# Optimization experiments

Measured on AMD Instinct MI355X. Metric: run time of the kernel, lower is better.

## Reference

```python
import jax, jax.numpy as jnp
import numpy as np

N, E, F, H, HEADS, L, G, NC = 50000, 800000, 128, 64, 4, 3, 64, 2
EPS = 1e-5


def _init(key, shape, fan_in):
    return jax.random.normal(key, shape, jnp.float32) / np.sqrt(fan_in)


def setup_inputs() -> dict:
    key = jax.random.key(0)
    ks = jax.random.split(key, 24)
    x = jax.random.normal(ks[0], (N, F), jnp.float32)
    edge_index = jax.random.randint(ks[1], (2, E), 0, N, jnp.int32)
    batch = jnp.sort(jax.random.randint(ks[2], (N,), 0, G, jnp.int32))
    return {
        "x": x, "edge_index": edge_index, "batch": batch,
        "Wi": _init(ks[3], (F, H), F), "bi": jnp.zeros((H,), jnp.float32),
        "gcn_W": _init(ks[4], (L, H, H), H), "gcn_b": jnp.zeros((L, H), jnp.float32),
        "gcn_gamma": jnp.ones((L, H), jnp.float32), "gcn_beta": jnp.zeros((L, H), jnp.float32),
        "Wg": _init(ks[5], (H, HEADS * H), H), "bg": jnp.zeros((H,), jnp.float32),
        "att_src": _init(ks[6], (HEADS, H), H), "att_dst": _init(ks[7], (HEADS, H), H),
        "gat_gamma": jnp.ones((H,), jnp.float32), "gat_beta": jnp.zeros((H,), jnp.float32),
        "c1_W": _init(ks[8], (2 * H, H), 2 * H), "c1_b": jnp.zeros((H,), jnp.float32),
        "c2_W": _init(ks[9], (H, H // 2), H), "c2_b": jnp.zeros((H // 2,), jnp.float32),
        "c3_W": _init(ks[10], (H // 2, NC), H // 2), "c3_b": jnp.zeros((NC,), jnp.float32),
    }


def _batch_norm(x, gamma, beta):
    # training-mode BN over the node dimension
    mu = x.mean(0)
    var = x.var(0)
    return (x - mu) * jax.lax.rsqrt(var + EPS) * gamma + beta


def _gcn_conv(x, W, b, src, dst):
    # PyG GCNConv: add self loops + symmetric normalization D^-1/2 (A+I) D^-1/2
    h = x @ W  # [N, H]
    ones = jnp.ones((src.shape[0],), h.dtype)
    deg = jax.ops.segment_sum(ones, dst, num_segments=N) + 1.0  # +1 for self loop
    dinv = jax.lax.rsqrt(deg)
    norm = dinv[src] * dinv[dst]  # [E]
    out = jax.ops.segment_sum(h[src] * norm[:, None], dst, num_segments=N)
    out = out + h * (dinv * dinv)[:, None]  # self-loop term: deg^-1
    return out + b


def _gat_conv(x, W, att_s, att_d, b, src, dst):
    # PyG GATConv, concat=False (mean over heads), leaky_relu slope 0.2, self loops
    h = (x @ W).reshape(N, HEADS, H)  # [N, Hd, C]
    a_s = (h * att_s).sum(-1)  # [N, Hd]
    a_d = (h * att_d).sum(-1)
    sl = jnp.arange(N, dtype=src.dtype)
    si = jnp.concatenate([src, sl])
    di = jnp.concatenate([dst, sl])
    logits = jax.nn.leaky_relu(a_s[si] + a_d[di], 0.2)  # [E+N, Hd]
    # segment softmax over destination node per head
    m = jax.ops.segment_max(logits, di, num_segments=N)  # every node has a self loop
    e = jnp.exp(logits - m[di])
    s = jax.ops.segment_sum(e, di, num_segments=N)
    alpha = e / (s[di] + 1e-16)  # [E+N, Hd]
    out = jax.ops.segment_sum(h[si] * alpha[:, :, None], di, num_segments=N)  # [N, Hd, C]
    return out.mean(axis=1) + b


def reference(x, edge_index, batch, Wi, bi, gcn_W, gcn_b, gcn_gamma, gcn_beta,
              Wg, bg, att_src, att_dst, gat_gamma, gat_beta,
              c1_W, c1_b, c2_W, c2_b, c3_W, c3_b):
    src, dst = edge_index[0], edge_index[1]
    h = jax.nn.relu(x @ Wi + bi)
    for l in range(L):
        identity = h
        h = _gcn_conv(h, gcn_W[l], gcn_b[l], src, dst)
        h = _batch_norm(h, gcn_gamma[l], gcn_beta[l])
        h = jax.nn.relu(h)  # dropout: eval mode (identity)
        h = h + identity
    identity = h
    h = _gat_conv(h, Wg, att_src, att_dst, bg, src, dst)
    h = _batch_norm(h, gat_gamma, gat_beta)
    h = jax.nn.elu(h)
    h = h + identity
    # dual pooling over graphs
    cnt = jax.ops.segment_sum(jnp.ones((N,), h.dtype), batch, num_segments=G,
                              indices_are_sorted=True)
    x_mean = jax.ops.segment_sum(h, batch, num_segments=G, indices_are_sorted=True)
    x_mean = x_mean / jnp.maximum(cnt, 1.0)[:, None]
    x_max = jax.ops.segment_max(h, batch, num_segments=G, indices_are_sorted=True)
    x_max = jnp.where(jnp.isfinite(x_max), x_max, 0.0)
    z = jnp.concatenate([x_mean, x_max], axis=1)  # [G, 2H]
    z = jax.nn.relu(z @ c1_W + c1_b)
    z = jax.nn.relu(z @ c2_W + c2_b)
    return z @ c3_W + c3_b  # [G, NC]
```

## Files before the change

kernel.cpp:

```cpp
#include <hip/hip_runtime.h>
#include <math.h>

#define N_ 50000
#define E_ 800000
#define F_ 128
#define H_ 64
#define G_ 64
#define NC_ 2
#define CAP_ 96
#define EPS_ 1e-5f
#define GRID_P 1250
#define GRID_G 2048
#define WIS_STRIDE 136
#define W0_STRIDE 72
#define WGS 72

typedef _Float16 f16;
typedef f16 f16x2 __attribute__((ext_vector_type(2)));
typedef f16 f16x4 __attribute__((ext_vector_type(4)));
typedef f16 f16x8 __attribute__((ext_vector_type(8)));

__device__ __forceinline__ unsigned fkey(float f) {
    unsigned u = __float_as_uint(f);
    return (u & 0x80000000u) ? ~u : (u | 0x80000000u);
}
__device__ __forceinline__ float funkey(unsigned k) {
    unsigned u = (k & 0x80000000u) ? (k & 0x7fffffffu) : ~k;
    return __uint_as_float(u);
}
__device__ __forceinline__ float leaky(float x) { return x > 0.f ? x : 0.2f * x; }

__device__ __forceinline__ void dot8(const f16x8 w, const f16x8 v,
                                     float& a0, float& a1, float& a2, float& a3) {
    a0 = __builtin_amdgcn_fdot2(__builtin_shufflevector(w, w, 0, 1),
                                __builtin_shufflevector(v, v, 0, 1), a0, false);
    a1 = __builtin_amdgcn_fdot2(__builtin_shufflevector(w, w, 2, 3),
                                __builtin_shufflevector(v, v, 2, 3), a1, false);
    a2 = __builtin_amdgcn_fdot2(__builtin_shufflevector(w, w, 4, 5),
                                __builtin_shufflevector(v, v, 4, 5), a2, false);
    a3 = __builtin_amdgcn_fdot2(__builtin_shufflevector(w, w, 6, 7),
                                __builtin_shufflevector(v, v, 6, 7), a3, false);
}

__device__ __forceinline__ int sel4(int4 v, int i) {
    return i == 0 ? v.x : i == 1 ? v.y : i == 2 ? v.z : v.w;
}

__global__ void k_fill(const int* __restrict__ ei, int* __restrict__ rowcnt,
                       int* __restrict__ slotS) {
    int e = blockIdx.x * 256 + threadIdx.x;
    if (e >= E_) return;
    int d = ei[E_ + e];
    int pos = atomicAdd(&rowcnt[d], 1);
    if (pos < CAP_) slotS[d * CAP_ + pos] = ei[e];
}

__global__ __launch_bounds__(256) void k_in_mm(const float* __restrict__ x,
                                               const float* __restrict__ Wi,
                                               const float* __restrict__ bi,
                                               const float* __restrict__ W0,
                                               const int* __restrict__ rowcnt,
                                               float* __restrict__ hA,
                                               f16* __restrict__ hWs) {
    __shared__ __attribute__((aligned(16))) f16 Wis[H_ * WIS_STRIDE];
    __shared__ __attribute__((aligned(16))) f16 W0s[H_ * W0_STRIDE];
    __shared__ __attribute__((aligned(16))) f16 xb[4 * F_];
    __shared__ __attribute__((aligned(16))) f16 rb[4 * H_];
    int tid = threadIdx.x;
    for (int i = tid; i < F_ * H_; i += 256) {
        int k = i >> 6, j = i & 63;
        Wis[j * WIS_STRIDE + k] = (f16)Wi[i];
    }
    for (int i = tid; i < H_ * H_; i += 256) {
        int k = i >> 6, j = i & 63;
        W0s[j * W0_STRIDE + k] = (f16)W0[i];
    }
    __syncthreads();
    int r = tid >> 6, j = tid & 63;
    float bj = bi[j];
    const f16* wc1 = Wis + j * WIS_STRIDE;
    const f16* wc2 = W0s + j * W0_STRIDE;
    f16* xr = xb + r * F_;
    f16* rr = rb + r * H_;
    int grp = blockIdx.x;
    float2 xv = *(const float2*)&x[(size_t)(grp * 4 + r) * F_ + 2 * j];
    for (; grp < N_ / 4; grp += GRID_P) {
        f16x2 xs = {(f16)xv.x, (f16)xv.y};
        *(f16x2*)&xr[2 * j] = xs;
        int ng = grp + GRID_P;
        if (ng < N_ / 4)
            xv = *(const float2*)&x[(size_t)(ng * 4 + r) * F_ + 2 * j];
        int n = grp * 4 + r;
        float a0 = 0.f, a1 = 0.f, a2 = 0.f, a3 = 0.f;
#pragma unroll
        for (int k = 0; k < F_; k += 8)
            dot8(*(const f16x8*)&wc1[k], *(const f16x8*)&xr[k], a0, a1, a2, a3);
        float y = fmaxf((a0 + a1) + (a2 + a3) + bj, 0.f);
        hA[(size_t)n * H_ + j] = y;
        rr[j] = (f16)y;
        float b0 = 0.f, b1 = 0.f, b2 = 0.f, b3 = 0.f;
#pragma unroll
        for (int k = 0; k < H_; k += 8)
            dot8(*(const f16x8*)&wc2[k], *(const f16x8*)&rr[k], b0, b1, b2, b3);
        hWs[(size_t)n * H_ + j] =
            (f16)(((b0 + b1) + (b2 + b3)) * rsqrtf((float)rowcnt[n] + 1.f));
    }
}

__global__ __launch_bounds__(256) void k_gcn_gather(const int* __restrict__ rowcnt,
                                                    const int* __restrict__ slotS,
                                                    const f16* __restrict__ hWs,
                                                    float* __restrict__ out,
                                                    float* __restrict__ bnpart) {
    __shared__ float st[128];
    for (int i = threadIdx.x; i < 128; i += 256) st[i] = 0.f;
    __syncthreads();
    int L = threadIdx.x & 63;
    int rg = L >> 4, q = L & 15;
    for (int grp = blockIdx.x; grp < N_ / 4; grp += GRID_G) {
        int d = grp * 4 + (threadIdx.x >> 6);
        int rc = rowcnt[d];
        int cnt = min(rc, CAP_);
        float dd = rsqrtf((float)rc + 1.f);
        size_t base = (size_t)d * CAP_;
        float a0 = 0.f, a1 = 0.f, a2 = 0.f, a3 = 0.f;
        if (rg == 0) {
            f16x4 hv = *(const f16x4*)&hWs[(size_t)d * H_ + q * 4];
            a0 = (float)hv[0]; a1 = (float)hv[1]; a2 = (float)hv[2]; a3 = (float)hv[3];
        }
        for (int k = 0; k < cnt; k += 16) {
            int4 iA = *(const int4*)&slotS[base + k];
            int4 iB = *(const int4*)&slotS[base + k + 4];
            int4 iC = *(const int4*)&slotS[base + k + 8];
            int4 iD = *(const int4*)&slotS[base + k + 12];
            int e = k + rg;
            int s0 = (e < cnt) ? sel4(iA, rg) : d;
            int s1 = (e + 4 < cnt) ? sel4(iB, rg) : d;
            int s2 = (e + 8 < cnt) ? sel4(iC, rg) : d;
            int s3 = (e + 12 < cnt) ? sel4(iD, rg) : d;
            f16x4 v0 = *(const f16x4*)&hWs[(size_t)s0 * H_ + q * 4];
            f16x4 v1 = *(const f16x4*)&hWs[(size_t)s1 * H_ + q * 4];
            f16x4 v2 = *(const f16x4*)&hWs[(size_t)s2 * H_ + q * 4];
            f16x4 v3 = *(const f16x4*)&hWs[(size_t)s3 * H_ + q * 4];
            float m0 = (e < cnt) ? 1.f : 0.f;
            float m1 = (e + 4 < cnt) ? 1.f : 0.f;
            float m2 = (e + 8 < cnt) ? 1.f : 0.f;
            float m3 = (e + 12 < cnt) ? 1.f : 0.f;
            a0 += (m0 * (float)v0[0] + m1 * (float)v1[0]) +
                  (m2 * (float)v2[0] + m3 * (float)v3[0]);
            a1 += (m0 * (float)v0[1] + m1 * (float)v1[1]) +
                  (m2 * (float)v2[1] + m3 * (float)v3[1]);
            a2 += (m0 * (float)v0[2] + m1 * (float)v1[2]) +
                  (m2 * (float)v2[2] + m3 * (float)v3[2]);
            a3 += (m0 * (float)v0[3] + m1 * (float)v1[3]) +
                  (m2 * (float)v2[3] + m3 * (float)v3[3]);
        }
        a0 += __shfl_xor(a0, 16); a0 += __shfl_xor(a0, 32);
        a1 += __shfl_xor(a1, 16); a1 += __shfl_xor(a1, 32);
        a2 += __shfl_xor(a2, 16); a2 += __shfl_xor(a2, 32);
        a3 += __shfl_xor(a3, 16); a3 += __shfl_xor(a3, 32);
        if (rg == 0) {
            float y0 = a0 * dd, y1 = a1 * dd, y2 = a2 * dd, y3 = a3 * dd;
            *(float4*)&out[(size_t)d * H_ + q * 4] = make_float4(y0, y1, y2, y3);
            atomicAdd(&st[q * 4 + 0], y0);        atomicAdd(&st[64 + q * 4 + 0], y0 * y0);
            atomicAdd(&st[q * 4 + 1], y1);        atomicAdd(&st[64 + q * 4 + 1], y1 * y1);
            atomicAdd(&st[q * 4 + 2], y2);        atomicAdd(&st[64 + q * 4 + 2], y2 * y2);
            atomicAdd(&st[q * 4 + 3], y3);        atomicAdd(&st[64 + q * 4 + 3], y3 * y3);
        }
    }
    __syncthreads();
    for (int i = threadIdx.x; i < 128; i += 256)
        atomicAdd(&bnpart[(blockIdx.x & 255) * 128 + i], st[i]);
}

__global__ void k_bn_final(const float* __restrict__ part, float* __restrict__ stat) {
    int t = threadIdx.x;
    float s = 0.f;
    for (int b = 0; b < 256; b++) s += part[b * 128 + t];
    __shared__ float red[128];
    red[t] = s;
    __syncthreads();
    if (t < H_) {
        float mu = red[t] / (float)N_;
        float var = red[H_ + t] / (float)N_ - mu * mu;
        stat[t] = mu;
        stat[H_ + t] = rsqrtf(var + EPS_);
    }
}

__global__ __launch_bounds__(256) void k_bn_mm(const float* __restrict__ v,
                                               const float* __restrict__ stat,
                                               const float* __restrict__ gamma,
                                               const float* __restrict__ beta,
                                               const float* __restrict__ res,
                                               const float* __restrict__ W,
                                               const int* __restrict__ rowcnt,
                                               float* __restrict__ out_res,
                                               f16* __restrict__ hWs) {
    __shared__ __attribute__((aligned(16))) f16 Ws[H_ * W0_STRIDE];
    __shared__ __attribute__((aligned(16))) f16 rb[4 * H_];
    int tid = threadIdx.x;
    for (int i = tid; i < H_ * H_; i += 256) {
        int k = i >> 6, j = i & 63;
        Ws[j * W0_STRIDE + k] = (f16)W[i];
    }
    __syncthreads();
    int r = tid >> 6, j = tid & 63;
    float mu = stat[j], rs = stat[H_ + j], ga = gamma[j], be = beta[j];
    const f16* wc = Ws + j * W0_STRIDE;
    f16* rr = rb + r * H_;
    for (int grp = blockIdx.x; grp < N_ / 4; grp += GRID_P) {
        int n = grp * 4 + r;
        size_t idx = (size_t)n * H_ + j;
        float y = (v[idx] - mu) * rs * ga + be;
        y = fmaxf(y, 0.f) + res[idx];
        out_res[idx] = y;
        rr[j] = (f16)y;
        float b0 = 0.f, b1 = 0.f, b2 = 0.f, b3 = 0.f;
#pragma unroll
        for (int k = 0; k < H_; k += 8)
            dot8(*(const f16x8*)&wc[k], *(const f16x8*)&rr[k], b0, b1, b2, b3);
        hWs[idx] = (f16)(((b0 + b1) + (b2 + b3)) * rsqrtf((float)rowcnt[n] + 1.f));
    }
}

__global__ __launch_bounds__(256) void k_wg(const float* __restrict__ v,
                                            const float* __restrict__ stat,
                                            const float* __restrict__ gamma,
                                            const float* __restrict__ beta,
                                            const float* __restrict__ res,
                                            const float* __restrict__ Wg,
                                            const float* __restrict__ asw,
                                            const float* __restrict__ adw,
                                            float* __restrict__ hOut,
                                            f16* __restrict__ hg16,
                                            float* __restrict__ a_s,
                                            float* __restrict__ a_d) {
    __shared__ __attribute__((aligned(16))) f16 Wgs[256 * WGS];
    __shared__ __attribute__((aligned(16))) f16 xb[32 * H_];
    int tid = threadIdx.x;
    for (int i = tid; i < H_ * 256; i += 256) {
        int k = i >> 8, j = i & 255;
        Wgs[j * WGS + k] = (f16)Wg[i];
    }
    int n0 = blockIdx.x * 32;
    int nrows = min(32, N_ - n0);
    {
        int c = tid & 63;
        float mu = stat[c], rs = stat[H_ + c], ga = gamma[c], be = beta[c];
        for (int i = tid; i < nrows * H_; i += 256) {
            size_t idx = (size_t)n0 * H_ + i;
            float y = (v[idx] - mu) * rs * ga + be;
            y = fmaxf(y, 0.f) + res[idx];
            hOut[idx] = y;
            xb[i] = (f16)y;
        }
    }
    __syncthreads();
    int j = tid, wid = j >> 6, lane = j & 63;
    float aw = asw[j], dw = adw[j];
    const f16* wcol = &Wgs[j * WGS];
    for (int nn = 0; nn < nrows; nn++) {
        const f16* hr = xb + nn * H_;
        float a0 = 0.f, a1 = 0.f, a2 = 0.f, a3 = 0.f;
#pragma unroll
        for (int k = 0; k < H_; k += 8)
            dot8(*(const f16x8*)&wcol[k], *(const f16x8*)&hr[k], a0, a1, a2, a3);
        float acc = (a0 + a1) + (a2 + a3);
        int n = n0 + nn;
        hg16[(size_t)n * 256 + j] = (f16)acc;
        float ps = acc * aw, pd = acc * dw;
        for (int m = 1; m < 64; m <<= 1) {
            ps += __shfl_xor(ps, m);
            pd += __shfl_xor(pd, m);
        }
        if (lane == 0) { a_s[n * 4 + wid] = ps; a_d[n * 4 + wid] = pd; }
    }
}

#define GAT_LOAD(sfx, KK)                                                      \
    {                                                                          \
        int4 iA = *(const int4*)&slotS[base + (KK)];                           \
        int4 iB = *(const int4*)&slotS[base + (KK) + 4];                       \
        s0##sfx = ((KK) + rg < cnt) ? (rg ? iA.y : iA.x) : d;                  \
        s1##sfx = ((KK) + 2 + rg < cnt) ? (rg ? iA.w : iA.z) : d;              \
        s2##sfx = ((KK) + 4 + rg < cnt) ? (rg ? iB.y : iB.x) : d;              \
        s3##sfx = ((KK) + 6 + rg < cnt) ? (rg ? iB.w : iB.z) : d;              \
        x0##sfx = a_s[s0##sfx * 4 + h];                                        \
        x1##sfx = a_s[s1##sfx * 4 + h];                                        \
        x2##sfx = a_s[s2##sfx * 4 + h];                                        \
        x3##sfx = a_s[s3##sfx * 4 + h];                                        \
        v0##sfx = *(const f16x8*)&hg16[(size_t)s0##sfx * 256 + p * 8];         \
        v1##sfx = *(const f16x8*)&hg16[(size_t)s1##sfx * 256 + p * 8];         \
        v2##sfx = *(const f16x8*)&hg16[(size_t)s2##sfx * 256 + p * 8];         \
        v3##sfx = *(const f16x8*)&hg16[(size_t)s3##sfx * 256 + p * 8];         \
    }

#define GAT_COMP(sfx, KK)                                                      \
    {                                                                          \
        float t0 = ((KK) + rg < cnt)                                           \
                       ? __expf(fminf(leaky(x0##sfx + ads), 19.f) - 8.f) : 0.f;\
        float t1 = ((KK) + 2 + rg < cnt)                                       \
                       ? __expf(fminf(leaky(x1##sfx + ads), 19.f) - 8.f) : 0.f;\
        float t2 = ((KK) + 4 + rg < cnt)                                       \
                       ? __expf(fminf(leaky(x2##sfx + ads), 19.f) - 8.f) : 0.f;\
        float t3 = ((KK) + 6 + rg < cnt)                                       \
                       ? __expf(fminf(leaky(x3##sfx + ads), 19.f) - 8.f) : 0.f;\
        s += (t0 + t1) + (t2 + t3);                                            \
        _Pragma("unroll")                                                      \
        for (int i = 0; i < 8; i++)                                            \
            acc[i] += (t0 * (float)v0##sfx[i] + t1 * (float)v1##sfx[i]) +      \
                      (t2 * (float)v2##sfx[i] + t3 * (float)v3##sfx[i]);       \
    }

__global__ __launch_bounds__(256) void k_gat(const int* __restrict__ rowcnt,
                                             const int* __restrict__ slotS,
                                             const f16* __restrict__ hg16,
                                             const float* __restrict__ a_s,
                                             const float* __restrict__ a_d,
                                             float* __restrict__ out,
                                             float* __restrict__ bnpart) {
    __shared__ float st[128];
    for (int i = threadIdx.x; i < 128; i += 256) st[i] = 0.f;
    __syncthreads();
    int L = threadIdx.x & 63;
    int rg = L >> 5, p = L & 31;
    int h = p >> 3, o = p & 7;
    for (int grp = blockIdx.x; grp < N_ / 4; grp += GRID_G) {
        int d = grp * 4 + (threadIdx.x >> 6);
        int cnt = min(rowcnt[d], CAP_);
        size_t base = (size_t)d * CAP_;
        float ads = a_d[d * 4 + h];
        float es = __expf(fminf(leaky(a_s[d * 4 + h] + ads), 19.f) - 8.f);
        float s = 0.f;
        float acc[8];
#pragma unroll
        for (int i = 0; i < 8; i++) acc[i] = 0.f;
        if (rg == 0) {
            s = es;
            f16x8 hv = *(const f16x8*)&hg16[(size_t)d * 256 + p * 8];
#pragma unroll
            for (int i = 0; i < 8; i++) acc[i] = es * (float)hv[i];
        }
        if (cnt > 0) {
            int s0A, s1A, s2A, s3A, s0B, s1B, s2B, s3B;
            float x0A, x1A, x2A, x3A, x0B, x1B, x2B, x3B;
            f16x8 v0A, v1A, v2A, v3A, v0B, v1B, v2B, v3B;
            GAT_LOAD(A, 0);
            int k = 0;
            for (; k + 8 < cnt; k += 16) {
                GAT_LOAD(B, k + 8);
                GAT_COMP(A, k);
                if (k + 16 < cnt) { GAT_LOAD(A, k + 16); }
                GAT_COMP(B, k + 8);
            }
            if (k < cnt) GAT_COMP(A, k);
        }
        s += __shfl_xor(s, 32);
#pragma unroll
        for (int i = 0; i < 8; i++) acc[i] += __shfl_xor(acc[i], 32);
        float w = 0.25f / (s + 1e-16f);
#pragma unroll
        for (int i = 0; i < 8; i++) acc[i] *= w;
#pragma unroll
        for (int i = 0; i < 8; i++) {
            acc[i] += __shfl_xor(acc[i], 8);
            acc[i] += __shfl_xor(acc[i], 16);
        }
        if (L < 8) {
            float4 oA = make_float4(acc[0], acc[1], acc[2], acc[3]);
            float4 oB = make_float4(acc[4], acc[5], acc[6], acc[7]);
            *(float4*)&out[(size_t)d * H_ + o * 8] = oA;
            *(float4*)&out[(size_t)d * H_ + o * 8 + 4] = oB;
#pragma unroll
            for (int i = 0; i < 8; i++) {
                atomicAdd(&st[o * 8 + i], acc[i]);
                atomicAdd(&st[64 + o * 8 + i], acc[i] * acc[i]);
            }
        }
    }
    __syncthreads();
    for (int i = threadIdx.x; i < 128; i += 256)
        atomicAdd(&bnpart[(blockIdx.x & 255) * 128 + i], st[i]);
}

__global__ __launch_bounds__(256) void k_pool_bn(const float* __restrict__ accv,
                                                 const float* __restrict__ stat,
                                                 const float* __restrict__ gamma,
                                                 const float* __restrict__ beta,
                                                 const float* __restrict__ res,
                                                 const int* __restrict__ batch,
                                                 float* __restrict__ xmean,
                                                 unsigned int* __restrict__ xmaxb,
                                                 float* __restrict__ cnt) {
    const int CH = 196;
    int n0 = blockIdx.x * CH;
    int nEnd = min(n0 + CH, N_);
    int c = threadIdx.x & 63, r = threadIdx.x >> 6;
    float mu = stat[c], rs = stat[H_ + c], ga = gamma[c], be = beta[c];
    int curg = -1, cc = 0;
    float s = 0.f;
    unsigned mk = 0u;
    for (int n = n0 + r; n < nEnd; n += 4) {
        int g = batch[n];
        if (g != curg) {
            if (curg >= 0) {
                atomicAdd(&xmean[curg * H_ + c], s);
                atomicMax(&xmaxb[curg * H_ + c], mk);
                if (c == 0) atomicAdd(&cnt[curg], (float)cc);
            }
            curg = g; s = 0.f; mk = 0u; cc = 0;
        }
        size_t idx = (size_t)n * H_ + c;
        float y = (accv[idx] - mu) * rs * ga + be;
        y = (y > 0.f ? y : expf(y) - 1.f) + res[idx];
        s += y;
        unsigned kv = fkey(y);
        mk = mk > kv ? mk : kv;
        cc++;
    }
    if (curg >= 0) {
        atomicAdd(&xmean[curg * H_ + c], s);
        atomicMax(&xmaxb[curg * H_ + c], mk);
        if (c == 0) atomicAdd(&cnt[curg], (float)cc);
    }
}

__global__ __launch_bounds__(64) void k_head(const float* __restrict__ xmean,
                                             const unsigned int* __restrict__ xmaxb,
                                             const float* __restrict__ cnt,
                                             const float* __restrict__ c1W, const float* __restrict__ c1b,
                                             const float* __restrict__ c2W, const float* __restrict__ c2b,
                                             const float* __restrict__ c3W, const float* __restrict__ c3b,
                                             float* __restrict__ out) {
    __shared__ float z[2 * H_];
    __shared__ float o1[H_];
    __shared__ float o2[32];
    int g = blockIdx.x, j = threadIdx.x;
    float cn = fmaxf(cnt[g], 1.f);
    z[j] = xmean[g * H_ + j] / cn;
    unsigned key = xmaxb[g * H_ + j];
    z[H_ + j] = (key == 0u) ? 0.f : funkey(key);
    __syncthreads();
    float a0 = c1b[j], a1 = 0.f, a2 = 0.f, a3 = 0.f;
    for (int k = 0; k < 2 * H_; k += 4) {
        a0 += z[k] * c1W[k * 64 + j];
        a1 += z[k + 1] * c1W[(k + 1) * 64 + j];
        a2 += z[k + 2] * c1W[(k + 2) * 64 + j];
        a3 += z[k + 3] * c1W[(k + 3) * 64 + j];
    }
    o1[j] = fmaxf((a0 + a1) + (a2 + a3), 0.f);
    __syncthreads();
    if (j < 32) {
        float b0 = c2b[j], b1 = 0.f, b2 = 0.f, b3 = 0.f;
        for (int k = 0; k < H_; k += 4) {
            b0 += o1[k] * c2W[k * 32 + j];
            b1 += o1[k + 1] * c2W[(k + 1) * 32 + j];
            b2 += o1[k + 2] * c2W[(k + 2) * 32 + j];
            b3 += o1[k + 3] * c2W[(k + 3) * 32 + j];
        }
        o2[j] = fmaxf((b0 + b1) + (b2 + b3), 0.f);
    }
    __syncthreads();
    if (j < NC_) {
        float c0 = c3b[j];
        for (int k = 0; k < 32; k++) c0 += o2[k] * c3W[k * 2 + j];
        out[g * NC_ + j] = c0;
    }
}

extern "C" void kernel_launch(void* const* d_in, const int* in_sizes, int n_in,
                              void* d_out, int out_size, void* d_ws, size_t ws_size,
                              hipStream_t stream) {
    const float* x     = (const float*)d_in[0];
    const int*   ei    = (const int*)d_in[1];
    const int*   batch = (const int*)d_in[2];
    const float* Wi    = (const float*)d_in[3];
    const float* bi    = (const float*)d_in[4];
    const float* gcnW  = (const float*)d_in[5];
    const float* gcnG  = (const float*)d_in[7];
    const float* gcnB  = (const float*)d_in[8];
    const float* Wg    = (const float*)d_in[9];
    const float* attS  = (const float*)d_in[11];
    const float* attD  = (const float*)d_in[12];
    const float* gatG  = (const float*)d_in[13];
    const float* gatB  = (const float*)d_in[14];
    const float* c1W   = (const float*)d_in[15];
    const float* c1b   = (const float*)d_in[16];
    const float* c2W   = (const float*)d_in[17];
    const float* c2b   = (const float*)d_in[18];
    const float* c3W   = (const float*)d_in[19];
    const float* c3b   = (const float*)d_in[20];
    float* out = (float*)d_out;

    float* p = (float*)d_ws;
    float* hA    = p; p += (size_t)N_ * H_;
    float* hB    = p; p += (size_t)N_ * H_;
    float* acc   = p; p += (size_t)N_ * H_;
    f16*   hg16  = (f16*)p; p += (size_t)N_ * 128;
    float* a_s   = p; p += (size_t)N_ * 4;
    float* a_d   = p; p += (size_t)N_ * 4;
    float* bnstat = p; p += 2 * H_;
    float* xmean  = p; p += G_ * H_;
    unsigned int* xmaxb = (unsigned int*)p; p += G_ * H_;
    float* cnt = p; p += G_;
    int* rowcnt = (int*)p; p += N_;
    float* bnpart4 = p; p += 4 * 256 * 128;
    int* slotS = (int*)p; p += (size_t)N_ * CAP_ + 16;
    f16* hWs = (f16*)hg16;

    float* bnp0 = bnpart4;
    float* bnp1 = bnpart4 + 1 * 256 * 128;
    float* bnp2 = bnpart4 + 2 * 256 * 128;
    float* bnp3 = bnpart4 + 3 * 256 * 128;

    const int NB_E = (E_ + 255) / 256;

    hipMemsetAsync(rowcnt, 0, (N_ + 4 * 256 * 128) * sizeof(float), stream);
    k_fill<<<NB_E, 256, 0, stream>>>(ei, rowcnt, slotS);

    k_in_mm<<<GRID_P, 256, 0, stream>>>(x, Wi, bi, gcnW, rowcnt, hA, hWs);

    k_gcn_gather<<<GRID_G, 256, 0, stream>>>(rowcnt, slotS, hWs, acc, bnp0);
    k_bn_final<<<1, 128, 0, stream>>>(bnp0, bnstat);
    k_bn_mm<<<GRID_P, 256, 0, stream>>>(acc, bnstat, gcnG, gcnB, hA,
                                        gcnW + (size_t)1 * H_ * H_, rowcnt, hB, hWs);
    k_gcn_gather<<<GRID_G, 256, 0, stream>>>(rowcnt, slotS, hWs, acc, bnp1);
    k_bn_final<<<1, 128, 0, stream>>>(bnp1, bnstat);
    k_bn_mm<<<GRID_P, 256, 0, stream>>>(acc, bnstat, gcnG + H_, gcnB + H_, hB,
                                        gcnW + (size_t)2 * H_ * H_, rowcnt, hA, hWs);
    k_gcn_gather<<<GRID_G, 256, 0, stream>>>(rowcnt, slotS, hWs, acc, bnp2);
    k_bn_final<<<1, 128, 0, stream>>>(bnp2, bnstat);

    k_wg<<<(N_ + 31) / 32, 256, 0, stream>>>(acc, bnstat, gcnG + 2 * H_, gcnB + 2 * H_,
                                             hA, Wg, attS, attD, hB, hg16, a_s, a_d);
    k_gat<<<GRID_G, 256, 0, stream>>>(rowcnt, slotS, hg16, a_s, a_d, acc, bnp3);
    k_bn_final<<<1, 128, 0, stream>>>(bnp3, bnstat);

    hipMemsetAsync(xmean, 0, (G_ * H_ * 2 + G_) * sizeof(float), stream);
    k_pool_bn<<<256, 256, 0, stream>>>(acc, bnstat, gatG, gatB, hB, batch,
                                       xmean, xmaxb, cnt);

    k_head<<<G_, 64, 0, stream>>>(xmean, xmaxb, cnt, c1W, c1b, c2W, c2b, c3W, c3b, out);
}
```

Baseline: 523.8 us.

## Make k_wg persistent and give k_gat one block per four destination nodes

k_wg becomes a grid-stride persistent kernel with 768 blocks, so the Wg-to-shared f16 conversion is paid once per block instead of once per 32-row tile. k_gat drops its grid-stride loop and software-pipelined double-buffered loads in favour of one block per four destinations, a simple 8-edge loop and a scalar tail. Its shared-memory BN statistics now go to per-row slots summed once, replacing shared atomics. The trade is less memory-level parallelism per thread in the gather, with more resident blocks meant to hide latency instead.

```diff
diff --git a/kernel.cpp b/kernel.cpp
--- a/kernel.cpp
+++ b/kernel.cpp
@@ -11,6 +11,7 @@
 #define EPS_ 1e-5f
 #define GRID_P 1250
 #define GRID_G 2048
+#define GRID_W 768
 #define WIS_STRIDE 136
 #define W0_STRIDE 72
 #define WGS 72
@@ -243,11 +244,16 @@
         int k = i >> 8, j = i & 255;
         Wgs[j * WGS + k] = (f16)Wg[i];
     }
-    int n0 = blockIdx.x * 32;
-    int nrows = min(32, N_ - n0);
-    {
-        int c = tid & 63;
-        float mu = stat[c], rs = stat[H_ + c], ga = gamma[c], be = beta[c];
+    int c = tid & 63;
+    float mu = stat[c], rs = stat[H_ + c], ga = gamma[c], be = beta[c];
+    int j = tid, wid = j >> 6, lane = j & 63;
+    float aw = asw[j], dw = adw[j];
+    const f16* wcol = &Wgs[j * WGS];
+    const int NGRP = (N_ + 31) / 32;
+    for (int g0 = blockIdx.x; g0 < NGRP; g0 += GRID_W) {
+        int n0 = g0 * 32;
+        int nrows = min(32, N_ - n0);
+        __syncthreads();
         for (int i = tid; i < nrows * H_; i += 256) {
             size_t idx = (size_t)n0 * H_ + i;
             float y = (v[idx] - mu) * rs * ga + be;
@@ -255,63 +261,25 @@
             hOut[idx] = y;
             xb[i] = (f16)y;
         }
-    }
-    __syncthreads();
-    int j = tid, wid = j >> 6, lane = j & 63;
-    float aw = asw[j], dw = adw[j];
-    const f16* wcol = &Wgs[j * WGS];
-    for (int nn = 0; nn < nrows; nn++) {
-        const f16* hr = xb + nn * H_;
-        float a0 = 0.f, a1 = 0.f, a2 = 0.f, a3 = 0.f;
-#pragma unroll
-        for (int k = 0; k < H_; k += 8)
-            dot8(*(const f16x8*)&wcol[k], *(const f16x8*)&hr[k], a0, a1, a2, a3);
-        float acc = (a0 + a1) + (a2 + a3);
-        int n = n0 + nn;
-        hg16[(size_t)n * 256 + j] = (f16)acc;
-        float ps = acc * aw, pd = acc * dw;
-        for (int m = 1; m < 64; m <<= 1) {
-            ps += __shfl_xor(ps, m);
-            pd += __shfl_xor(pd, m);
-        }
-        if (lane == 0) { a_s[n * 4 + wid] = ps; a_d[n * 4 + wid] = pd; }
-    }
-}
-
-#define GAT_LOAD(sfx, KK)                                                      \
-    {                                                                          \
-        int4 iA = *(const int4*)&slotS[base + (KK)];                           \
-        int4 iB = *(const int4*)&slotS[base + (KK) + 4];                       \
-        s0##sfx = ((KK) + rg < cnt) ? (rg ? iA.y : iA.x) : d;                  \
-        s1##sfx = ((KK) + 2 + rg < cnt) ? (rg ? iA.w : iA.z) : d;              \
-        s2##sfx = ((KK) + 4 + rg < cnt) ? (rg ? iB.y : iB.x) : d;              \
-        s3##sfx = ((KK) + 6 + rg < cnt) ? (rg ? iB.w : iB.z) : d;              \
-        x0##sfx = a_s[s0##sfx * 4 + h];                                        \
-        x1##sfx = a_s[s1##sfx * 4 + h];                                        \
-        x2##sfx = a_s[s2##sfx * 4 + h];                                        \
-        x3##sfx = a_s[s3##sfx * 4 + h];                                        \
-        v0##sfx = *(const f16x8*)&hg16[(size_t)s0##sfx * 256 + p * 8];         \
-        v1##sfx = *(const f16x8*)&hg16[(size_t)s1##sfx * 256 + p * 8];         \
-        v2##sfx = *(const f16x8*)&hg16[(size_t)s2##sfx * 256 + p * 8];         \
-        v3##sfx = *(const f16x8*)&hg16[(size_t)s3##sfx * 256 + p * 8];         \
-    }
-
-#define GAT_COMP(sfx, KK)                                                      \
-    {                                                                          \
-        float t0 = ((KK) + rg < cnt)                                           \
-                       ? __expf(fminf(leaky(x0##sfx + ads), 19.f) - 8.f) : 0.f;\
-        float t1 = ((KK) + 2 + rg < cnt)                                       \
-                       ? __expf(fminf(leaky(x1##sfx + ads), 19.f) - 8.f) : 0.f;\
-        float t2 = ((KK) + 4 + rg < cnt)                                       \
-                       ? __expf(fminf(leaky(x2##sfx + ads), 19.f) - 8.f) : 0.f;\
-        float t3 = ((KK) + 6 + rg < cnt)                                       \
-                       ? __expf(fminf(leaky(x3##sfx + ads), 19.f) - 8.f) : 0.f;\
-        s += (t0 + t1) + (t2 + t3);                                            \
-        _Pragma("unroll")                                                      \
-        for (int i = 0; i < 8; i++)                                            \
-            acc[i] += (t0 * (float)v0##sfx[i] + t1 * (float)v1##sfx[i]) +      \
-                      (t2 * (float)v2##sfx[i] + t3 * (float)v3##sfx[i]);       \
-    }
+        __syncthreads();
+        for (int nn = 0; nn < nrows; nn++) {
+            const f16* hr = xb + nn * H_;
+            float a0 = 0.f, a1 = 0.f, a2 = 0.f, a3 = 0.f;
+#pragma unroll
+            for (int k = 0; k < H_; k += 8)
+                dot8(*(const f16x8*)&wcol[k], *(const f16x8*)&hr[k], a0, a1, a2, a3);
+            float acc = (a0 + a1) + (a2 + a3);
+            int n = n0 + nn;
+            hg16[(size_t)n * 256 + j] = (f16)acc;
+            float ps = acc * aw, pd = acc * dw;
+            for (int m = 1; m < 64; m <<= 1) {
+                ps += __shfl_xor(ps, m);
+                pd += __shfl_xor(pd, m);
+            }
+            if (lane == 0) { a_s[n * 4 + wid] = ps; a_d[n * 4 + wid] = pd; }
+        }
+    }
+}
 
 __global__ __launch_bounds__(256) void k_gat(const int* __restrict__ rowcnt,
                                              const int* __restrict__ slotS,
@@ -320,68 +288,89 @@
                                              const float* __restrict__ a_d,
                                              float* __restrict__ out,
                                              float* __restrict__ bnpart) {
-    __shared__ float st[128];
-    for (int i = threadIdx.x; i < 128; i += 256) st[i] = 0.f;
-    __syncthreads();
+    __shared__ float st[4][128];
+    int r = threadIdx.x >> 6;
+    int d = blockIdx.x * 4 + r;
     int L = threadIdx.x & 63;
     int rg = L >> 5, p = L & 31;
     int h = p >> 3, o = p & 7;
-    for (int grp = blockIdx.x; grp < N_ / 4; grp += GRID_G) {
-        int d = grp * 4 + (threadIdx.x >> 6);
-        int cnt = min(rowcnt[d], CAP_);
-        size_t base = (size_t)d * CAP_;
-        float ads = a_d[d * 4 + h];
-        float es = __expf(fminf(leaky(a_s[d * 4 + h] + ads), 19.f) - 8.f);
-        float s = 0.f;
-        float acc[8];
-#pragma unroll
-        for (int i = 0; i < 8; i++) acc[i] = 0.f;
-        if (rg == 0) {
-            s = es;
-            f16x8 hv = *(const f16x8*)&hg16[(size_t)d * 256 + p * 8];
-#pragma unroll
-            for (int i = 0; i < 8; i++) acc[i] = es * (float)hv[i];
-        }
-        if (cnt > 0) {
-            int s0A, s1A, s2A, s3A, s0B, s1B, s2B, s3B;
-            float x0A, x1A, x2A, x3A, x0B, x1B, x2B, x3B;
-            f16x8 v0A, v1A, v2A, v3A, v0B, v1B, v2B, v3B;
-            GAT_LOAD(A, 0);
-            int k = 0;
-            for (; k + 8 < cnt; k += 16) {
-                GAT_LOAD(B, k + 8);
-                GAT_COMP(A, k);
-                if (k + 16 < cnt) { GAT_LOAD(A, k + 16); }
-                GAT_COMP(B, k + 8);
-            }
-            if (k < cnt) GAT_COMP(A, k);
-        }
-        s += __shfl_xor(s, 32);
-#pragma unroll
-        for (int i = 0; i < 8; i++) acc[i] += __shfl_xor(acc[i], 32);
-        float w = 0.25f / (s + 1e-16f);
-#pragma unroll
-        for (int i = 0; i < 8; i++) acc[i] *= w;
+    int cnt = min(rowcnt[d], CAP_);
+    size_t base = (size_t)d * CAP_;
+    float ads = a_d[d * 4 + h];
+    float es = __expf(fminf(leaky(a_s[d * 4 + h] + ads), 19.f) - 8.f);
+    float s = 0.f;
+    float acc[8];
+#pragma unroll
+    for (int i = 0; i < 8; i++) acc[i] = 0.f;
+    if (rg == 0) {
+        s = es;
+        f16x8 hv = *(const f16x8*)&hg16[(size_t)d * 256 + p * 8];
+#pragma unroll
+        for (int i = 0; i < 8; i++) acc[i] = es * (float)hv[i];
+    }
+    int k = 0;
+    for (; k + 8 <= cnt; k += 8) {
+        int4 sA = *(const int4*)&slotS[base + k];
+        int4 sB = *(const int4*)&slotS[base + k + 4];
+        int s0 = rg ? sA.y : sA.x;
+        int s1 = rg ? sA.w : sA.z;
+        int s2 = rg ? sB.y : sB.x;
+        int s3 = rg ? sB.w : sB.z;
+        float x0 = a_s[s0 * 4 + h];
+        float x1 = a_s[s1 * 4 + h];
+        float x2 = a_s[s2 * 4 + h];
+        float x3 = a_s[s3 * 4 + h];
+        f16x8 v0 = *(const f16x8*)&hg16[(size_t)s0 * 256 + p * 8];
+        f16x8 v1 = *(const f16x8*)&hg16[(size_t)s1 * 256 + p * 8];
+        f16x8 v2 = *(const f16x8*)&hg16[(size_t)s2 * 256 + p * 8];
+        f16x8 v3 = *(const f16x8*)&hg16[(size_t)s3 * 256 + p * 8];
+        float t0 = __expf(fminf(leaky(x0 + ads), 19.f) - 8.f);
+        float t1 = __expf(fminf(leaky(x1 + ads), 19.f) - 8.f);
+        float t2 = __expf(fminf(leaky(x2 + ads), 19.f) - 8.f);
+        float t3 = __expf(fminf(leaky(x3 + ads), 19.f) - 8.f);
+        s += (t0 + t1) + (t2 + t3);
+#pragma unroll
+        for (int i = 0; i < 8; i++)
+            acc[i] += (t0 * (float)v0[i] + t1 * (float)v1[i]) +
+                      (t2 * (float)v2[i] + t3 * (float)v3[i]);
+    }
+    for (; k < cnt; k += 2) {
+        if (k + rg < cnt) {
+            int sE = slotS[base + k + rg];
+            float t = __expf(fminf(leaky(a_s[sE * 4 + h] + ads), 19.f) - 8.f);
+            f16x8 v = *(const f16x8*)&hg16[(size_t)sE * 256 + p * 8];
+            s += t;
+#pragma unroll
+            for (int i = 0; i < 8; i++) acc[i] += t * (float)v[i];
+        }
+    }
+    s += __shfl_xor(s, 32);
+#pragma unroll
+    for (int i = 0; i < 8; i++) acc[i] += __shfl_xor(acc[i], 32);
+    float w = 0.25f / (s + 1e-16f);
+#pragma unroll
+    for (int i = 0; i < 8; i++) acc[i] *= w;
+#pragma unroll
+    for (int i = 0; i < 8; i++) {
+        acc[i] += __shfl_xor(acc[i], 8);
+        acc[i] += __shfl_xor(acc[i], 16);
+    }
+    if (L < 8) {
+        float4 oA = make_float4(acc[0], acc[1], acc[2], acc[3]);
+        float4 oB = make_float4(acc[4], acc[5], acc[6], acc[7]);
+        *(float4*)&out[(size_t)d * H_ + o * 8] = oA;
+        *(float4*)&out[(size_t)d * H_ + o * 8 + 4] = oB;
 #pragma unroll
         for (int i = 0; i < 8; i++) {
-            acc[i] += __shfl_xor(acc[i], 8);
-            acc[i] += __shfl_xor(acc[i], 16);
-        }
-        if (L < 8) {
-            float4 oA = make_float4(acc[0], acc[1], acc[2], acc[3]);
-            float4 oB = make_float4(acc[4], acc[5], acc[6], acc[7]);
-            *(float4*)&out[(size_t)d * H_ + o * 8] = oA;
-            *(float4*)&out[(size_t)d * H_ + o * 8 + 4] = oB;
-#pragma unroll
-            for (int i = 0; i < 8; i++) {
-                atomicAdd(&st[o * 8 + i], acc[i]);
-                atomicAdd(&st[64 + o * 8 + i], acc[i] * acc[i]);
-            }
-        }
-    }
-    __syncthreads();
-    for (int i = threadIdx.x; i < 128; i += 256)
-        atomicAdd(&bnpart[(blockIdx.x & 255) * 128 + i], st[i]);
+            st[r][o * 8 + i] = acc[i];
+            st[r][64 + o * 8 + i] = acc[i] * acc[i];
+        }
+    }
+    __syncthreads();
+    for (int t = threadIdx.x; t < 128; t += 256) {
+        float vsum = (st[0][t] + st[1][t]) + (st[2][t] + st[3][t]);
+        atomicAdd(&bnpart[(blockIdx.x & 255) * 128 + t], vsum);
+    }
 }
 
 __global__ __launch_bounds__(256) void k_pool_bn(const float* __restrict__ accv,
@@ -515,6 +504,7 @@
     float* bnp3 = bnpart4 + 3 * 256 * 128;
 
     const int NB_E = (E_ + 255) / 256;
+    const int NB_W = N_ / 4;
 
     hipMemsetAsync(rowcnt, 0, (N_ + 4 * 256 * 128) * sizeof(float), stream);
     k_fill<<<NB_E, 256, 0, stream>>>(ei, rowcnt, slotS);
@@ -532,9 +522,9 @@
     k_gcn_gather<<<GRID_G, 256, 0, stream>>>(rowcnt, slotS, hWs, acc, bnp2);
     k_bn_final<<<1, 128, 0, stream>>>(bnp2, bnstat);
 
-    k_wg<<<(N_ + 31) / 32, 256, 0, stream>>>(acc, bnstat, gcnG + 2 * H_, gcnB + 2 * H_,
-                                             hA, Wg, attS, attD, hB, hg16, a_s, a_d);
-    k_gat<<<GRID_G, 256, 0, stream>>>(rowcnt, slotS, hg16, a_s, a_d, acc, bnp3);
+    k_wg<<<GRID_W, 256, 0, stream>>>(acc, bnstat, gcnG + 2 * H_, gcnB + 2 * H_,
+                                     hA, Wg, attS, attD, hB, hg16, a_s, a_d);
+    k_gat<<<NB_W, 256, 0, stream>>>(rowcnt, slotS, hg16, a_s, a_d, acc, bnp3);
     k_bn_final<<<1, 128, 0, stream>>>(bnp3, bnstat);
 
     hipMemsetAsync(xmean, 0, (G_ * H_ * 2 + G_) * sizeof(float), stream);
```

After: 529.6 us. About the same (+1.1%).

## Store neighbor slots as 16-bit indices and launch one block per node group

Applied to the files above, without the earlier changes.

The padded neighbor-slot table now stores source indices as unsigned 16-bit values instead of 32-bit ints. This is valid because the node count is below 65536, and it halves the index bytes fetched by the GCN and GAT gather kernels. The gather kernels also drop the grid-stride loop: they launch one block per four destination nodes and replace the shared-memory float atomics for batch-norm statistics with per-row slots reduced after a barrier. In exchange, the number of global atomicAdd calls into the per-block partial buffer rises about sixfold, and launch count per kernel grows.

```diff
diff --git a/kernel.cpp b/kernel.cpp
--- a/kernel.cpp
+++ b/kernel.cpp
@@ -10,7 +10,6 @@
 #define CAP_ 96
 #define EPS_ 1e-5f
 #define GRID_P 1250
-#define GRID_G 2048
 #define WIS_STRIDE 136
 #define W0_STRIDE 72
 #define WGS 72
@@ -19,6 +18,8 @@
 typedef f16 f16x2 __attribute__((ext_vector_type(2)));
 typedef f16 f16x4 __attribute__((ext_vector_type(4)));
 typedef f16 f16x8 __attribute__((ext_vector_type(8)));
+typedef unsigned short u16;
+typedef u16 u16x8 __attribute__((ext_vector_type(8)));
 
 __device__ __forceinline__ unsigned fkey(float f) {
     unsigned u = __float_as_uint(f);
@@ -42,17 +43,13 @@
                                 __builtin_shufflevector(v, v, 6, 7), a3, false);
 }
 
-__device__ __forceinline__ int sel4(int4 v, int i) {
-    return i == 0 ? v.x : i == 1 ? v.y : i == 2 ? v.z : v.w;
-}
-
 __global__ void k_fill(const int* __restrict__ ei, int* __restrict__ rowcnt,
-                       int* __restrict__ slotS) {
+                       u16* __restrict__ slotS) {
     int e = blockIdx.x * 256 + threadIdx.x;
     if (e >= E_) return;
     int d = ei[E_ + e];
     int pos = atomicAdd(&rowcnt[d], 1);
-    if (pos < CAP_) slotS[d * CAP_ + pos] = ei[e];
+    if (pos < CAP_) slotS[d * CAP_ + pos] = (u16)ei[e];
 }
 
 __global__ __launch_bounds__(256) void k_in_mm(const float* __restrict__ x,
@@ -108,69 +105,66 @@
 }
 
 __global__ __launch_bounds__(256) void k_gcn_gather(const int* __restrict__ rowcnt,
-                                                    const int* __restrict__ slotS,
+                                                    const u16* __restrict__ slotS,
                                                     const f16* __restrict__ hWs,
                                                     float* __restrict__ out,
                                                     float* __restrict__ bnpart) {
-    __shared__ float st[128];
-    for (int i = threadIdx.x; i < 128; i += 256) st[i] = 0.f;
-    __syncthreads();
+    __shared__ float st[4][128];
+    int r = threadIdx.x >> 6;
+    int d = blockIdx.x * 4 + r;
     int L = threadIdx.x & 63;
     int rg = L >> 4, q = L & 15;
-    for (int grp = blockIdx.x; grp < N_ / 4; grp += GRID_G) {
-        int d = grp * 4 + (threadIdx.x >> 6);
-        int rc = rowcnt[d];
-        int cnt = min(rc, CAP_);
-        float dd = rsqrtf((float)rc + 1.f);
-        size_t base = (size_t)d * CAP_;
-        float a0 = 0.f, a1 = 0.f, a2 = 0.f, a3 = 0.f;
-        if (rg == 0) {
-            f16x4 hv = *(const f16x4*)&hWs[(size_t)d * H_ + q * 4];
-            a0 = (float)hv[0]; a1 = (float)hv[1]; a2 = (float)hv[2]; a3 = (float)hv[3];
-        }
-        for (int k = 0; k < cnt; k += 16) {
-            int4 iA = *(const int4*)&slotS[base + k];
-            int4 iB = *(const int4*)&slotS[base + k + 4];
-            int4 iC = *(const int4*)&slotS[base + k + 8];
-            int4 iD = *(const int4*)&slotS[base + k + 12];
-            int e = k + rg;
-            int s0 = (e < cnt) ? sel4(iA, rg) : d;
-            int s1 = (e + 4 < cnt) ? sel4(iB, rg) : d;
-            int s2 = (e + 8 < cnt) ? sel4(iC, rg) : d;
-            int s3 = (e + 12 < cnt) ? sel4(iD, rg) : d;
-            f16x4 v0 = *(const f16x4*)&hWs[(size_t)s0 * H_ + q * 4];
-            f16x4 v1 = *(const f16x4*)&hWs[(size_t)s1 * H_ + q * 4];
-            f16x4 v2 = *(const f16x4*)&hWs[(size_t)s2 * H_ + q * 4];
-            f16x4 v3 = *(const f16x4*)&hWs[(size_t)s3 * H_ + q * 4];
-            float m0 = (e < cnt) ? 1.f : 0.f;
-            float m1 = (e + 4 < cnt) ? 1.f : 0.f;
-            float m2 = (e + 8 < cnt) ? 1.f : 0.f;
-            float m3 = (e + 12 < cnt) ? 1.f : 0.f;
-            a0 += (m0 * (float)v0[0] + m1 * (float)v1[0]) +
-                  (m2 * (float)v2[0] + m3 * (float)v3[0]);
-            a1 += (m0 * (float)v0[1] + m1 * (float)v1[1]) +
-                  (m2 * (float)v2[1] + m3 * (float)v3[1]);
-            a2 += (m0 * (float)v0[2] + m1 * (float)v1[2]) +
-                  (m2 * (float)v2[2] + m3 * (float)v3[2]);
-            a3 += (m0 * (float)v0[3] + m1 * (float)v1[3]) +
-                  (m2 * (float)v2[3] + m3 * (float)v3[3]);
-        }
-        a0 += __shfl_xor(a0, 16); a0 += __shfl_xor(a0, 32);
-        a1 += __shfl_xor(a1, 16); a1 += __shfl_xor(a1, 32);
-        a2 += __shfl_xor(a2, 16); a2 += __shfl_xor(a2, 32);
-        a3 += __shfl_xor(a3, 16); a3 += __shfl_xor(a3, 32);
-        if (rg == 0) {
-            float y0 = a0 * dd, y1 = a1 * dd, y2 = a2 * dd, y3 = a3 * dd;
-            *(float4*)&out[(size_t)d * H_ + q * 4] = make_float4(y0, y1, y2, y3);
-            atomicAdd(&st[q * 4 + 0], y0);        atomicAdd(&st[64 + q * 4 + 0], y0 * y0);
-            atomicAdd(&st[q * 4 + 1], y1);        atomicAdd(&st[64 + q * 4 + 1], y1 * y1);
-            atomicAdd(&st[q * 4 + 2], y2);        atomicAdd(&st[64 + q * 4 + 2], y2 * y2);
-            atomicAdd(&st[q * 4 + 3], y3);        atomicAdd(&st[64 + q * 4 + 3], y3 * y3);
-        }
-    }
-    __syncthreads();
-    for (int i = threadIdx.x; i < 128; i += 256)
-        atomicAdd(&bnpart[(blockIdx.x & 255) * 128 + i], st[i]);
+    int rc = rowcnt[d];
+    int cnt = min(rc, CAP_);
+    float dd = rsqrtf((float)rc + 1.f);
+    size_t base = (size_t)d * CAP_;
+    float a0 = 0.f, a1 = 0.f, a2 = 0.f, a3 = 0.f;
+    if (rg == 0) {
+        f16x4 hv = *(const f16x4*)&hWs[(size_t)d * H_ + q * 4];
+        a0 = (float)hv[0]; a1 = (float)hv[1]; a2 = (float)hv[2]; a3 = (float)hv[3];
+    }
+    for (int k = 0; k < cnt; k += 16) {
+        u16x8 iA = *(const u16x8*)&slotS[base + k];
+        u16x8 iB = *(const u16x8*)&slotS[base + k + 8];
+        int e = k + rg;
+        int s0 = (e < cnt) ? (int)iA[rg] : d;
+        int s1 = (e + 4 < cnt) ? (int)iA[4 + rg] : d;
+        int s2 = (e + 8 < cnt) ? (int)iB[rg] : d;
+        int s3 = (e + 12 < cnt) ? (int)iB[4 + rg] : d;
+        f16x4 v0 = *(const f16x4*)&hWs[(size_t)s0 * H_ + q * 4];
+        f16x4 v1 = *(const f16x4*)&hWs[(size_t)s1 * H_ + q * 4];
+        f16x4 v2 = *(const f16x4*)&hWs[(size_t)s2 * H_ + q * 4];
+        f16x4 v3 = *(const f16x4*)&hWs[(size_t)s3 * H_ + q * 4];
+        float m0 = (e < cnt) ? 1.f : 0.f;
+        float m1 = (e + 4 < cnt) ? 1.f : 0.f;
+        float m2 = (e + 8 < cnt) ? 1.f : 0.f;
+        float m3 = (e + 12 < cnt) ? 1.f : 0.f;
+        a0 += (m0 * (float)v0[0] + m1 * (float)v1[0]) +
+              (m2 * (float)v2[0] + m3 * (float)v3[0]);
+        a1 += (m0 * (float)v0[1] + m1 * (float)v1[1]) +
+              (m2 * (float)v2[1] + m3 * (float)v3[1]);
+        a2 += (m0 * (float)v0[2] + m1 * (float)v1[2]) +
+              (m2 * (float)v2[2] + m3 * (float)v3[2]);
+        a3 += (m0 * (float)v0[3] + m1 * (float)v1[3]) +
+              (m2 * (float)v2[3] + m3 * (float)v3[3]);
+    }
+    a0 += __shfl_xor(a0, 16); a0 += __shfl_xor(a0, 32);
+    a1 += __shfl_xor(a1, 16); a1 += __shfl_xor(a1, 32);
+    a2 += __shfl_xor(a2, 16); a2 += __shfl_xor(a2, 32);
+    a3 += __shfl_xor(a3, 16); a3 += __shfl_xor(a3, 32);
+    if (rg == 0) {
+        float y0 = a0 * dd, y1 = a1 * dd, y2 = a2 * dd, y3 = a3 * dd;
+        *(float4*)&out[(size_t)d * H_ + q * 4] = make_float4(y0, y1, y2, y3);
+        st[r][q * 4 + 0] = y0;  st[r][64 + q * 4 + 0] = y0 * y0;
+        st[r][q * 4 + 1] = y1;  st[r][64 + q * 4 + 1] = y1 * y1;
+        st[r][q * 4 + 2] = y2;  st[r][64 + q * 4 + 2] = y2 * y2;
+        st[r][q * 4 + 3] = y3;  st[r][64 + q * 4 + 3] = y3 * y3;
+    }
+    __syncthreads();
+    for (int t = threadIdx.x; t < 128; t += 256) {
+        float vsum = (st[0][t] + st[1][t]) + (st[2][t] + st[3][t]);
+        atomicAdd(&bnpart[(blockIdx.x & 255) * 128 + t], vsum);
+    }
 }
 
 __global__ void k_bn_final(const float* __restrict__ part, float* __restrict__ stat) {
@@ -280,12 +274,11 @@
 
 #define GAT_LOAD(sfx, KK)                                                      \
     {                                                                          \
-        int4 iA = *(const int4*)&slotS[base + (KK)];                           \
-        int4 iB = *(const int4*)&slotS[base + (KK) + 4];                       \
-        s0##sfx = ((KK) + rg < cnt) ? (rg ? iA.y : iA.x) : d;                  \
-        s1##sfx = ((KK) + 2 + rg < cnt) ? (rg ? iA.w : iA.z) : d;              \
-        s2##sfx = ((KK) + 4 + rg < cnt) ? (rg ? iB.y : iB.x) : d;              \
-        s3##sfx = ((KK) + 6 + rg < cnt) ? (rg ? iB.w : iB.z) : d;              \
+        u16x8 iA = *(const u16x8*)&slotS[base + (KK)];                         \
+        s0##sfx = ((KK) + rg < cnt) ? (int)iA[rg] : d;                         \
+        s1##sfx = ((KK) + 2 + rg < cnt) ? (int)iA[2 + rg] : d;                 \
+        s2##sfx = ((KK) + 4 + rg < cnt) ? (int)iA[4 + rg] : d;                 \
+        s3##sfx = ((KK) + 6 + rg < cnt) ? (int)iA[6 + rg] : d;                 \
         x0##sfx = a_s[s0##sfx * 4 + h];                                        \
         x1##sfx = a_s[s1##sfx * 4 + h];                                        \
         x2##sfx = a_s[s2##sfx * 4 + h];                                        \
@@ -314,74 +307,73 @@
     }
 
 __global__ __launch_bounds__(256) void k_gat(const int* __restrict__ rowcnt,
-                                             const int* __restrict__ slotS,
+                                             const u16* __restrict__ slotS,
                                              const f16* __restrict__ hg16,
                                              const float* __restrict__ a_s,
                                              const float* __restrict__ a_d,
                                              float* __restrict__ out,
                                              float* __restrict__ bnpart) {
-    __shared__ float st[128];
-    for (int i = threadIdx.x; i < 128; i += 256) st[i] = 0.f;
-    __syncthreads();
+    __shared__ float st[4][128];
+    int r = threadIdx.x >> 6;
+    int d = blockIdx.x * 4 + r;
     int L = threadIdx.x & 63;
     int rg = L >> 5, p = L & 31;
     int h = p >> 3, o = p & 7;
-    for (int grp = blockIdx.x; grp < N_ / 4; grp += GRID_G) {
-        int d = grp * 4 + (threadIdx.x >> 6);
-        int cnt = min(rowcnt[d], CAP_);
-        size_t base = (size_t)d * CAP_;
-        float ads = a_d[d * 4 + h];
-        float es = __expf(fminf(leaky(a_s[d * 4 + h] + ads), 19.f) - 8.f);
-        float s = 0.f;
-        float acc[8];
-#pragma unroll
-        for (int i = 0; i < 8; i++) acc[i] = 0.f;
-        if (rg == 0) {
-            s = es;
-            f16x8 hv = *(const f16x8*)&hg16[(size_t)d * 256 + p * 8];
-#pragma unroll
-            for (int i = 0; i < 8; i++) acc[i] = es * (float)hv[i];
+    int cnt = min(rowcnt[d], CAP_);
+    size_t base = (size_t)d * CAP_;
+    float ads = a_d[d * 4 + h];
+    float es = __expf(fminf(leaky(a_s[d * 4 + h] + ads), 19.f) - 8.f);
+    float s = 0.f;
+    float acc[8];
+#pragma unroll
+    for (int i = 0; i < 8; i++) acc[i] = 0.f;
+    if (rg == 0) {
+        s = es;
+        f16x8 hv = *(const f16x8*)&hg16[(size_t)d * 256 + p * 8];
+#pragma unroll
+        for (int i = 0; i < 8; i++) acc[i] = es * (float)hv[i];
+    }
+    if (cnt > 0) {
+        int s0A, s1A, s2A, s3A, s0B, s1B, s2B, s3B;
+        float x0A, x1A, x2A, x3A, x0B, x1B, x2B, x3B;
+        f16x8 v0A, v1A, v2A, v3A, v0B, v1B, v2B, v3B;
+        GAT_LOAD(A, 0);
+        int k = 0;
+        for (; k + 8 < cnt; k += 16) {
+            GAT_LOAD(B, k + 8);
+            GAT_COMP(A, k);
+            if (k + 16 < cnt) { GAT_LOAD(A, k + 16); }
+            GAT_COMP(B, k + 8);
         }
-        if (cnt > 0) {
-            int s0A, s1A, s2A, s3A, s0B, s1B, s2B, s3B;
-            float x0A, x1A, x2A, x3A, x0B, x1B, x2B, x3B;
-            f16x8 v0A, v1A, v2A, v3A, v0B, v1B, v2B, v3B;
-            GAT_LOAD(A, 0);
-            int k = 0;
-            for (; k + 8 < cnt; k += 16) {
-                GAT_LOAD(B, k + 8);
-                GAT_COMP(A, k);
-                if (k + 16 < cnt) { GAT_LOAD(A, k + 16); }
-                GAT_COMP(B, k + 8);
-            }
-            if (k < cnt) GAT_COMP(A, k);
+        if (k < cnt) GAT_COMP(A, k);
+    }
+    s += __shfl_xor(s, 32);
+#pragma unroll
+    for (int i = 0; i < 8; i++) acc[i] += __shfl_xor(acc[i], 32);
+    float w = 0.25f / (s + 1e-16f);
+#pragma unroll
+    for (int i = 0; i < 8; i++) acc[i] *= w;
+#pragma unroll
+    for (int i = 0; i < 8; i++) {
+        acc[i] += __shfl_xor(acc[i], 8);
+        acc[i] += __shfl_xor(acc[i], 16);
+    }
+    if (L < 8) {
+        float4 oA = make_float4(acc[0], acc[1], acc[2], acc[3]);
+        float4 oB = make_float4(acc[4], acc[5], acc[6], acc[7]);
+        *(float4*)&out[(size_t)d * H_ + o * 8] = oA;
+        *(float4*)&out[(size_t)d * H_ + o * 8 + 4] = oB;
+#pragma unroll
+        for (int i = 0; i < 8; i++) {
+            st[r][o * 8 + i] = acc[i];
+            st[r][64 + o * 8 + i] = acc[i] * acc[i];
         }
-        s += __shfl_xor(s, 32);
-#pragma unroll
-        for (int i = 0; i < 8; i++) acc[i] += __shfl_xor(acc[i], 32);
-        float w = 0.25f / (s + 1e-16f);
-#pragma unroll
-        for (int i = 0; i < 8; i++) acc[i] *= w;
-#pragma unroll
-        for (int i = 0; i < 8; i++) {
-            acc[i] += __shfl_xor(acc[i], 8);
-            acc[i] += __shfl_xor(acc[i], 16);
-        }
-        if (L < 8) {
-            float4 oA = make_float4(acc[0], acc[1], acc[2], acc[3]);
-            float4 oB = make_float4(acc[4], acc[5], acc[6], acc[7]);
-            *(float4*)&out[(size_t)d * H_ + o * 8] = oA;
-            *(float4*)&out[(size_t)d * H_ + o * 8 + 4] = oB;
-#pragma unroll
-            for (int i = 0; i < 8; i++) {
-                atomicAdd(&st[o * 8 + i], acc[i]);
-                atomicAdd(&st[64 + o * 8 + i], acc[i] * acc[i]);
-            }
-        }
-    }
-    __syncthreads();
-    for (int i = threadIdx.x; i < 128; i += 256)
-        atomicAdd(&bnpart[(blockIdx.x & 255) * 128 + i], st[i]);
+    }
+    __syncthreads();
+    for (int t = threadIdx.x; t < 128; t += 256) {
+        float vsum = (st[0][t] + st[1][t]) + (st[2][t] + st[3][t]);
+        atomicAdd(&bnpart[(blockIdx.x & 255) * 128 + t], vsum);
+    }
 }
 
 __global__ __launch_bounds__(256) void k_pool_bn(const float* __restrict__ accv,
@@ -506,7 +498,7 @@
     float* cnt = p; p += G_;
     int* rowcnt = (int*)p; p += N_;
     float* bnpart4 = p; p += 4 * 256 * 128;
-    int* slotS = (int*)p; p += (size_t)N_ * CAP_ + 16;
+    u16* slotS = (u16*)p; p += (size_t)N_ * CAP_ / 2 + 8;
     f16* hWs = (f16*)hg16;
 
     float* bnp0 = bnpart4;
@@ -515,26 +507,27 @@
     float* bnp3 = bnpart4 + 3 * 256 * 128;
 
     const int NB_E = (E_ + 255) / 256;
+    const int NB_W = N_ / 4;
 
     hipMemsetAsync(rowcnt, 0, (N_ + 4 * 256 * 128) * sizeof(float), stream);
     k_fill<<<NB_E, 256, 0, stream>>>(ei, rowcnt, slotS);
 
     k_in_mm<<<GRID_P, 256, 0, stream>>>(x, Wi, bi, gcnW, rowcnt, hA, hWs);
 
-    k_gcn_gather<<<GRID_G, 256, 0, stream>>>(rowcnt, slotS, hWs, acc, bnp0);
+    k_gcn_gather<<<NB_W, 256, 0, stream>>>(rowcnt, slotS, hWs, acc, bnp0);
     k_bn_final<<<1, 128, 0, stream>>>(bnp0, bnstat);
     k_bn_mm<<<GRID_P, 256, 0, stream>>>(acc, bnstat, gcnG, gcnB, hA,
                                         gcnW + (size_t)1 * H_ * H_, rowcnt, hB, hWs);
-    k_gcn_gather<<<GRID_G, 256, 0, stream>>>(rowcnt, slotS, hWs, acc, bnp1);
+    k_gcn_gather<<<NB_W, 256, 0, stream>>>(rowcnt, slotS, hWs, acc, bnp1);
     k_bn_final<<<1, 128, 0, stream>>>(bnp1, bnstat);
     k_bn_mm<<<GRID_P, 256, 0, stream>>>(acc, bnstat, gcnG + H_, gcnB + H_, hB,
                                         gcnW + (size_t)2 * H_ * H_, rowcnt, hA, hWs);
-    k_gcn_gather<<<GRID_G, 256, 0, stream>>>(rowcnt, slotS, hWs, acc, bnp2);
+    k_gcn_gather<<<NB_W, 256, 0, stream>>>(rowcnt, slotS, hWs, acc, bnp2);
     k_bn_final<<<1, 128, 0, stream>>>(bnp2, bnstat);
 
     k_wg<<<(N_ + 31) / 32, 256, 0, stream>>>(acc, bnstat, gcnG + 2 * H_, gcnB + 2 * H_,
                                              hA, Wg, attS, attD, hB, hg16, a_s, a_d);
-    k_gat<<<GRID_G, 256, 0, stream>>>(rowcnt, slotS, hg16, a_s, a_d, acc, bnp3);
+    k_gat<<<NB_W, 256, 0, stream>>>(rowcnt, slotS, hg16, a_s, a_d, acc, bnp3);
     k_bn_final<<<1, 128, 0, stream>>>(bnp3, bnstat);
 
     hipMemsetAsync(xmean, 0, (G_ * H_ * 2 + G_) * sizeof(float), stream);
```

New measurement: 458.7 us. 12.4% less time.
